# Kernel tuning notes

Measured on AMD Instinct MI355X. Metric: run time of the kernel, lower is better.

Reference implementation:

```python
import jax, jax.numpy as jnp
import numpy as np

B, T, I, H = 128, 2048, 256, 256


def setup_inputs() -> dict:
    key = jax.random.key(0)
    k1, k2, k3 = jax.random.split(key, 3)
    # xavier-uniform-like scale for weights
    s_x = float(np.sqrt(6.0 / (I + H)))
    s_h = float(np.sqrt(6.0 / (H + H)))
    return {
        "x": jax.random.normal(k1, (B, T, I), dtype=jnp.float32),
        "w_x": jax.random.uniform(k2, (I, H), jnp.float32, -s_x, s_x),
        "b_x": jnp.zeros((H,), jnp.float32),
        "w_h": jax.random.uniform(k3, (H, H), jnp.float32, -s_h, s_h),
        "b_h": jnp.zeros((H,), jnp.float32),
    }


def reference(x, w_x, b_x, w_h, b_h):
    # The original computes identical pre-activations for all four gates:
    # z = x_t @ w_x + b_x + h @ w_h + b_h; f=i=o=sigmoid(z), g=tanh(z).
    # Precompute the input projection for all timesteps in one GEMM.
    b, t, _ = x.shape
    h0 = jnp.zeros((b, w_h.shape[0]), x.dtype)
    c0 = jnp.zeros_like(h0)
    xproj = jnp.einsum('bti,ih->tbh', x, w_x) + b_x  # [T, B, H]

    def step(carry, xp_t):
        h, c = carry
        z = xp_t + h @ w_h + b_h
        s = jax.nn.sigmoid(z)   # f_t == i_t == o_t
        g = jnp.tanh(z)         # g_t
        c_new = s * c + s * g
        h_new = s * jnp.tanh(c_new)
        return (h_new, c_new), None

    (h_t, c_t), _ = jax.lax.scan(step, (h0, c0), xproj)
    return (h_t, c_t)
```

## Files before the change

kernel.cpp:

```cpp
#include <hip/hip_runtime.h>
#include <stdint.h>

#define B_ 128
#define T_ 2048
#define I_ 256
#define H_ 256


__device__ __forceinline__ void gates_sg(float z, float& s, float& g){
  float az = fabsf(z);
  float a  = __expf(-az);
  float r1 = __builtin_amdgcn_rcpf(1.0f + a);
  s = (z >= 0.0f) ? r1 : a * r1;
  float a2 = a * a;
  float gm = (1.0f - a2) * __builtin_amdgcn_rcpf(1.0f + a2);
  g = (z >= 0.0f) ? gm : -gm;
}
__device__ __forceinline__ float tanh_stable(float c){
  float ac = fabsf(c);
  float u  = __expf(-2.0f * ac);
  float tm = (1.0f - u) * __builtin_amdgcn_rcpf(1.0f + u);
  return (c >= 0.0f) ? tm : -tm;
}

__device__ __forceinline__ float bcast_lane(float v, int srclane){
  return __builtin_bit_cast(float,
      __builtin_amdgcn_readlane(__builtin_bit_cast(int, v), srclane));
}

template<int CTRL>
__device__ __forceinline__ float dpp_qperm(float v){
  return __builtin_bit_cast(float,
      __builtin_amdgcn_update_dpp(0, __builtin_bit_cast(int, v), CTRL, 0xF, 0xF, true));
}

#define FMA4(hs, wv, ax, ay, az, aw)            \
  ax = fmaf(hs, wv.x, ax); ay = fmaf(hs, wv.y, ay); \
  az = fmaf(hs, wv.z, az); aw = fmaf(hs, wv.w, aw);

#define PIN4(v) asm volatile("" : "+v"(v.x), "+v"(v.y), "+v"(v.z), "+v"(v.w))


__global__ __launch_bounds__(512, 2) void xproj_k(
    const float* __restrict__ x, const float* __restrict__ w_x,
    const float* __restrict__ b_x, const float* __restrict__ b_h,
    float* __restrict__ xp, int t0c, int Tc)
{
  const int tid  = threadIdx.x;
  const int wv   = tid >> 6;
  const int lane = tid & 63;
  const int ks   = wv * 32;

  float4 w4[32];
  #pragma unroll
  for (int kk = 0; kk < 32; ++kk)
    w4[kk] = *(const float4*)&w_x[(ks + kk) * H_ + 4 * lane];

  float bias = 0.0f;
  if (tid < 256) bias = b_x[tid] + b_h[tid];

  __shared__ float4 xs4[256];
  __shared__ float  pb[8][4][256];

  const int rows_per_b = Tc >> 2;
  const int nblk  = (B_ * Tc) >> 2;
  const int iters = (nblk + gridDim.x - 1) / gridDim.x;
  const int bid0  = blockIdx.x * iters;

  float4 r = make_float4(0,0,0,0);
  if (tid < 256 && bid0 < nblk){
    const int b  = bid0 / rows_per_b;
    const int t4 = (bid0 - b * rows_per_b) << 2;
    r = ((const float4*)x)[ (int64_t)(b * T_ + t0c + t4) * 64 + tid ];
  }

  for (int i = 0; i < iters; ++i){
    const int bid = bid0 + i;
    const bool valid = bid < nblk;
    if (tid < 256 && valid) xs4[tid] = r;
    __syncthreads();
    if (tid < 256 && bid + 1 < nblk){
      const int bn = bid + 1;
      const int b  = bn / rows_per_b;
      const int t4 = (bn - b * rows_per_b) << 2;
      r = ((const float4*)x)[ (int64_t)(b * T_ + t0c + t4) * 64 + tid ];
    }
    if (valid){
      #pragma unroll
      for (int rr = 0; rr < 4; ++rr){
        const float4* xr = &xs4[rr * 64 + (ks >> 2)];
        float ax = 0.f, ay = 0.f, az = 0.f, aw = 0.f;
        #pragma unroll
        for (int q = 0; q < 8; ++q){
          float4 hv = xr[q];
          FMA4(hv.x, w4[4*q+0], ax, ay, az, aw);
          FMA4(hv.y, w4[4*q+1], ax, ay, az, aw);
          FMA4(hv.z, w4[4*q+2], ax, ay, az, aw);
          FMA4(hv.w, w4[4*q+3], ax, ay, az, aw);
        }
        *(float4*)&pb[wv][rr][4*lane] = make_float4(ax, ay, az, aw);
      }
    }
    __syncthreads();
    if (valid && tid < 256){
      const int b  = bid / rows_per_b;
      const int t4 = (bid - b * rows_per_b) << 2;
      float z0 = bias, z1 = bias, z2 = bias, z3 = bias;
      #pragma unroll
      for (int w = 0; w < 8; ++w){
        z0 += pb[w][0][tid]; z1 += pb[w][1][tid];
        z2 += pb[w][2][tid]; z3 += pb[w][3][tid];
      }
      *(float4*)&xp[ ((int64_t)b * H_ + tid) * Tc + t4 ] = make_float4(z0, z1, z2, z3);
    }
  }
}


__global__ __launch_bounds__(1024, 4) void rec_k(
    const float* __restrict__ xp, const float* __restrict__ w_h,
    float* __restrict__ out, int Tc, int init)
{
  const int tid = threadIdx.x;
  const int w   = tid >> 6;
  const int l   = tid & 63;
  const int g   = l & 3;
  const int cq  = l >> 2;
  const int col = w * 16 + cq;
  const int b   = blockIdx.x;

  float4 wreg[16];
  #pragma unroll
  for (int kk = 0; kk < 16; ++kk)
    wreg[kk] = *(const float4*)&w_h[(16 * w + kk) * H_ + 4 * l];
  #pragma unroll
  for (int kk = 0; kk < 16; ++kk) PIN4(wreg[kk]);

  __shared__ float pbuf[2][16][260];

  float c = 0.f, hcur = 0.f;
  if (!init){
    hcur = out[(int64_t)b * H_ + col];
    c    = out[(int64_t)B_ * H_ + (int64_t)b * H_ + col];
  }

  const float* xpr = xp + ((int64_t)b * H_ + col) * Tc;
  float4 xq = *(const float4*)xpr;

  int pp = 0;
  for (int t = 0; t < Tc; t += 4){
    float xa[4] = {xq.x, xq.y, xq.z, xq.w};
    if (t + 4 < Tc) xq = *(const float4*)(xpr + t + 4);
    #pragma unroll
    for (int tt = 0; tt < 4; ++tt){
      float ax = 0.f, ay = 0.f, az = 0.f, aw = 0.f;
      #pragma unroll
      for (int kk = 0; kk < 16; ++kk){
        float hk = bcast_lane(hcur, 4 * kk);
        FMA4(hk, wreg[kk], ax, ay, az, aw);
      }
      *(float4*)&pbuf[pp][w][4 * l] = make_float4(ax, ay, az, aw);
      __syncthreads();
      float sum = (pbuf[pp][4*g+0][col] + pbuf[pp][4*g+1][col])
                + (pbuf[pp][4*g+2][col] + pbuf[pp][4*g+3][col]);
      sum += dpp_qperm<0xB1>(sum);
      sum += dpp_qperm<0x4E>(sum);
      float z = xa[tt] + sum;
      float s, gg; gates_sg(z, s, gg);
      c    = s * (c + gg);
      hcur = s * tanh_stable(c);
      pp ^= 1;
    }
  }
  if (g == 0){
    out[(int64_t)b * H_ + col] = hcur;
    out[(int64_t)B_ * H_ + (int64_t)b * H_ + col] = c;
  }
}


__global__ __launch_bounds__(512, 2) void lstm_fused_k(
    const float* __restrict__ x, const float* __restrict__ w_x,
    const float* __restrict__ b_x, const float* __restrict__ w_h,
    const float* __restrict__ b_h, float* __restrict__ out)
{
  const int tid  = threadIdx.x;
  const int wv   = tid >> 6;
  const int lane = tid & 63;
  const int ks   = wv * 32;
  const int b    = blockIdx.x;

  float4 wh4[32], wx4[32];
  #pragma unroll
  for (int kk = 0; kk < 32; ++kk){
    wh4[kk] = *(const float4*)&w_h[(ks + kk) * H_ + 4 * lane];
    wx4[kk] = *(const float4*)&w_x[(ks + kk) * H_ + 4 * lane];
  }
  float bias = 0.0f;
  if (tid < 256) bias = b_x[tid] + b_h[tid];

  __shared__ float hb[2][H_];
  __shared__ float4 xs4[2][64];
  __shared__ float pbuf[8][H_];
  const float* xrow = x + (int64_t)b * T_ * I_;
  if (tid < 256) hb[0][tid] = 0.f;
  if (tid < 64)  xs4[0][tid] = ((const float4*)xrow)[tid];
  __syncthreads();
  float c = 0.f, hn = 0.f;
  int p = 0;
  for (int t = 0; t < T_; ++t){
    const float4* hr = (const float4*)&hb[p][ks];
    const float4* xr = &xs4[p][ks >> 2];
    float ax = 0.f, ay = 0.f, az = 0.f, aw = 0.f;
    #pragma unroll
    for (int q = 0; q < 8; ++q){
      float4 hv = hr[q];
      FMA4(hv.x, wh4[4*q+0], ax, ay, az, aw);
      FMA4(hv.y, wh4[4*q+1], ax, ay, az, aw);
      FMA4(hv.z, wh4[4*q+2], ax, ay, az, aw);
      FMA4(hv.w, wh4[4*q+3], ax, ay, az, aw);
    }
    #pragma unroll
    for (int q = 0; q < 8; ++q){
      float4 xv = xr[q];
      FMA4(xv.x, wx4[4*q+0], ax, ay, az, aw);
      FMA4(xv.y, wx4[4*q+1], ax, ay, az, aw);
      FMA4(xv.z, wx4[4*q+2], ax, ay, az, aw);
      FMA4(xv.w, wx4[4*q+3], ax, ay, az, aw);
    }
    *(float4*)&pbuf[wv][4*lane] = make_float4(ax, ay, az, aw);
    __syncthreads();
    if (tid < 256){
      float z = bias
              + ((pbuf[0][tid] + pbuf[1][tid]) + (pbuf[2][tid] + pbuf[3][tid]))
              + ((pbuf[4][tid] + pbuf[5][tid]) + (pbuf[6][tid] + pbuf[7][tid]));
      float s, g; gates_sg(z, s, g);
      c  = s * (c + g);
      hn = s * tanh_stable(c);
      hb[p ^ 1][tid] = hn;
    } else if (tid < 320 && t + 1 < T_){
      xs4[p ^ 1][tid - 256] = ((const float4*)(xrow + (int64_t)(t + 1) * I_))[tid - 256];
    }
    __syncthreads();
    p ^= 1;
  }
  if (tid < 256){
    out[(int64_t)b * H_ + tid] = hn;
    out[(int64_t)B_ * H_ + (int64_t)b * H_ + tid] = c;
  }
}


extern "C" void kernel_launch(void* const* d_in, const int* in_sizes, int n_in,
                              void* d_out, int out_size, void* d_ws, size_t ws_size,
                              hipStream_t stream)
{
  const float* x   = (const float*)d_in[0];
  const float* w_x = (const float*)d_in[1];
  const float* b_x = (const float*)d_in[2];
  const float* w_h = (const float*)d_in[3];
  const float* b_h = (const float*)d_in[4];
  float* out = (float*)d_out;

  const size_t per_t = (size_t)B_ * H_ * sizeof(float);
  int Tc_max = (int)((ws_size / per_t) & ~(size_t)3);
  if (Tc_max >= 4){
    if (Tc_max > T_) Tc_max = T_;
    int done = 0, first = 1;
    while (done < T_){
      int Tc = (T_ - done < Tc_max) ? (T_ - done) : Tc_max;
      xproj_k<<<512, 512, 0, stream>>>(x, w_x, b_x, b_h, (float*)d_ws, done, Tc);
      rec_k<<<128, 1024, 0, stream>>>((const float*)d_ws, w_h, out, Tc, first);
      done += Tc; first = 0;
    }
  } else {
    lstm_fused_k<<<128, 512, 0, stream>>>(x, w_x, b_x, w_h, b_h, out);
  }
}
```

Before: 2.389 ms.

## Restructure recurrent kernel: two lanes per hidden column with LDS-broadcast h

The recurrent kernel now uses 512 threads where each pair of lanes owns one output column and splits the K dimension in halves. The hidden state is exchanged through a double-buffered shared array instead of readlane broadcasts plus a partial-sum buffer. Each step needs only one barrier and a single DPP add to combine the two halves. The goal is to shorten the per-timestep critical path by removing the cross-wave partial-sum reduction. In exchange it uses 128 weight registers per lane and does more LDS reads of h per step.

```diff
diff --git a/kernel.cpp b/kernel.cpp
--- a/kernel.cpp
+++ b/kernel.cpp
@@ -23,11 +23,6 @@
   return (c >= 0.0f) ? tm : -tm;
 }
 
-__device__ __forceinline__ float bcast_lane(float v, int srclane){
-  return __builtin_bit_cast(float,
-      __builtin_amdgcn_readlane(__builtin_bit_cast(int, v), srclane));
-}
-
 template<int CTRL>
 __device__ __forceinline__ float dpp_qperm(float v){
   return __builtin_bit_cast(float,
@@ -37,8 +32,6 @@
 #define FMA4(hs, wv, ax, ay, az, aw)            \
   ax = fmaf(hs, wv.x, ax); ay = fmaf(hs, wv.y, ay); \
   az = fmaf(hs, wv.z, az); aw = fmaf(hs, wv.w, aw);
-
-#define PIN4(v) asm volatile("" : "+v"(v.x), "+v"(v.y), "+v"(v.z), "+v"(v.w))
 
 
 __global__ __launch_bounds__(512, 2) void xproj_k(
@@ -117,34 +110,38 @@
 }
 
 
-__global__ __launch_bounds__(1024, 4) void rec_k(
+__global__ __launch_bounds__(512, 2) void rec_k(
     const float* __restrict__ xp, const float* __restrict__ w_h,
     float* __restrict__ out, int Tc, int init)
 {
   const int tid = threadIdx.x;
   const int w   = tid >> 6;
   const int l   = tid & 63;
-  const int g   = l & 3;
-  const int cq  = l >> 2;
-  const int col = w * 16 + cq;
+  const int s   = l & 1;
+  const int c   = 32 * w + (l >> 1);
   const int b   = blockIdx.x;
-
-  float4 wreg[16];
+  const int k0  = 128 * s;
+
+  float4 wreg[32];
   #pragma unroll
-  for (int kk = 0; kk < 16; ++kk)
-    wreg[kk] = *(const float4*)&w_h[(16 * w + kk) * H_ + 4 * l];
-  #pragma unroll
-  for (int kk = 0; kk < 16; ++kk) PIN4(wreg[kk]);
-
-  __shared__ float pbuf[2][16][260];
-
-  float c = 0.f, hcur = 0.f;
+  for (int q = 0; q < 32; ++q){
+    wreg[q].x = w_h[(k0 + 4*q + 0) * H_ + c];
+    wreg[q].y = w_h[(k0 + 4*q + 1) * H_ + c];
+    wreg[q].z = w_h[(k0 + 4*q + 2) * H_ + c];
+    wreg[q].w = w_h[(k0 + 4*q + 3) * H_ + c];
+  }
+
+  __shared__ float hlds[2][H_];
+
+  float cst = 0.f, hcur = 0.f;
   if (!init){
-    hcur = out[(int64_t)b * H_ + col];
-    c    = out[(int64_t)B_ * H_ + (int64_t)b * H_ + col];
-  }
-
-  const float* xpr = xp + ((int64_t)b * H_ + col) * Tc;
+    hcur = out[(int64_t)b * H_ + c];
+    cst  = out[(int64_t)B_ * H_ + (int64_t)b * H_ + c];
+  }
+  if (s == 0) hlds[0][c] = hcur;
+  __syncthreads();
+
+  const float* xpr = xp + ((int64_t)b * H_ + c) * Tc;
   float4 xq = *(const float4*)xpr;
 
   int pp = 0;
@@ -153,28 +150,30 @@
     if (t + 4 < Tc) xq = *(const float4*)(xpr + t + 4);
     #pragma unroll
     for (int tt = 0; tt < 4; ++tt){
+      const float4* h4 = (const float4*)&hlds[pp][k0];
       float ax = 0.f, ay = 0.f, az = 0.f, aw = 0.f;
       #pragma unroll
-      for (int kk = 0; kk < 16; ++kk){
-        float hk = bcast_lane(hcur, 4 * kk);
-        FMA4(hk, wreg[kk], ax, ay, az, aw);
+      for (int q = 0; q < 32; ++q){
+        float4 hv = h4[q];
+        ax = fmaf(hv.x, wreg[q].x, ax);
+        ay = fmaf(hv.y, wreg[q].y, ay);
+        az = fmaf(hv.z, wreg[q].z, az);
+        aw = fmaf(hv.w, wreg[q].w, aw);
       }
-      *(float4*)&pbuf[pp][w][4 * l] = make_float4(ax, ay, az, aw);
+      float sum = (ax + ay) + (az + aw);
+      sum += dpp_qperm<0xB1>(sum);
+      float z = xa[tt] + sum;
+      float sg, gg; gates_sg(z, sg, gg);
+      cst  = sg * (cst + gg);
+      hcur = sg * tanh_stable(cst);
+      if (s == 0) hlds[pp ^ 1][c] = hcur;
       __syncthreads();
-      float sum = (pbuf[pp][4*g+0][col] + pbuf[pp][4*g+1][col])
-                + (pbuf[pp][4*g+2][col] + pbuf[pp][4*g+3][col]);
-      sum += dpp_qperm<0xB1>(sum);
-      sum += dpp_qperm<0x4E>(sum);
-      float z = xa[tt] + sum;
-      float s, gg; gates_sg(z, s, gg);
-      c    = s * (c + gg);
-      hcur = s * tanh_stable(c);
       pp ^= 1;
     }
   }
-  if (g == 0){
-    out[(int64_t)b * H_ + col] = hcur;
-    out[(int64_t)B_ * H_ + (int64_t)b * H_ + col] = c;
+  if (s == 0){
+    out[(int64_t)b * H_ + c] = hcur;
+    out[(int64_t)B_ * H_ + (int64_t)b * H_ + c] = cst;
   }
 }
 
@@ -270,7 +269,7 @@
     while (done < T_){
       int Tc = (T_ - done < Tc_max) ? (T_ - done) : Tc_max;
       xproj_k<<<512, 512, 0, stream>>>(x, w_x, b_x, b_h, (float*)d_ws, done, Tc);
-      rec_k<<<128, 1024, 0, stream>>>((const float*)d_ws, w_h, out, Tc, first);
+      rec_k<<<128, 512, 0, stream>>>((const float*)d_ws, w_h, out, Tc, first);
       done += Tc; first = 0;
     }
   } else {
```

Result: slower. 3.113 ms (+30.3%).
